# Performance work log

Hardware: AMD Instinct MI355X
Metric: run time of the kernel (lower is better)

The kernel has to match this reference:

```python
import jax, jax.numpy as jnp
import numpy as np

B, C, IMG, P = 32, 3, 224, 16
D, H, L, F, NCLS = 768, 12, 12, 3072, 1000
NP = (IMG // P) ** 2  # 196
DH = D // H  # 64
EPS = 1e-5


def _ln(x, g, b):
    m = jnp.mean(x, axis=-1, keepdims=True)
    v = jnp.mean(jnp.square(x - m), axis=-1, keepdims=True)
    return (x - m) * jax.lax.rsqrt(v + EPS) * g + b


def setup_inputs() -> dict:
    key = jax.random.key(0)
    ks = iter(jax.random.split(key, 32))
    s = 0.02
    rn = lambda shape: jax.random.normal(next(ks), shape, dtype=jnp.float32) * s
    inp = {
        "x": jax.random.normal(next(ks), (B, C, IMG, IMG), dtype=jnp.float32),
        "Wp": rn((P * P * C, D)), "bp": jnp.zeros((D,), jnp.float32),
        "cls": rn((1, 1, D)), "pos": rn((1, NP + 1, D)),
        # per-layer stacked params (leading dim L)
        "ln1_g": jnp.ones((L, D), jnp.float32), "ln1_b": jnp.zeros((L, D), jnp.float32),
        "Wq": rn((L, H, D, DH)), "bq": jnp.zeros((L, H, DH), jnp.float32),
        "Wk": rn((L, H, D, DH)), "bk": jnp.zeros((L, H, DH), jnp.float32),
        "Wv": rn((L, H, D, DH)), "bv": jnp.zeros((L, H, DH), jnp.float32),
        "Wo": rn((L, D, D)), "bo": jnp.zeros((L, D), jnp.float32),
        "ln2_g": jnp.ones((L, D), jnp.float32), "ln2_b": jnp.zeros((L, D), jnp.float32),
        "W1": rn((L, D, F)), "b1": jnp.zeros((L, F), jnp.float32),
        "W2": rn((L, F, D)), "b2": jnp.zeros((L, D), jnp.float32),
        # classification head
        "hln_g": jnp.ones((D,), jnp.float32), "hln_b": jnp.zeros((D,), jnp.float32),
        "hW1": rn((D, D)), "hb1": jnp.zeros((D,), jnp.float32),
        "hW2": rn((D, NCLS)), "hb2": jnp.zeros((NCLS,), jnp.float32),
    }
    return inp


def _vit(x, Wp, bp, cls, pos, ln1_g, ln1_b, Wq, bq, Wk, bk, Wv, bv, Wo, bo,
         ln2_g, ln2_b, W1, b1, W2, b2, hln_g, hln_b, hW1, hb1, hW2, hb2):
    b = x.shape[0]
    g = IMG // P
    # nn.Unfold(k=16, s=16): channel order (c, kh, kw), patch order (ph, pw)
    patches = x.reshape(b, C, g, P, g, P).transpose(0, 2, 4, 1, 3, 5).reshape(b, NP, C * P * P)
    h = patches @ Wp + bp  # [b, NP, D]
    h = jnp.concatenate([jnp.broadcast_to(cls, (b, 1, D)), h], axis=1) + pos  # [b, S, D]

    scale = 1.0 / jnp.sqrt(jnp.asarray(DH, h.dtype))

    def step(h, p):
        g1, b1_, wq, bq_, wk, bk_, wv, bv_, wo, bo_, g2, b2_, w1, bb1, w2, bb2 = p
        xn = _ln(h, g1, b1_)
        q = jnp.einsum('bsd,hde->bhse', xn, wq) + bq_[:, None, :]
        k = jnp.einsum('bsd,hde->bhse', xn, wk) + bk_[:, None, :]
        v = jnp.einsum('bsd,hde->bhse', xn, wv) + bv_[:, None, :]
        scores = jnp.einsum('bhse,bhte->bhst', q, k) * scale
        attn = jax.nn.softmax(scores, axis=-1)
        o = jnp.einsum('bhst,bhte->bhse', attn, v)  # [b,H,S,DH]
        o = o.transpose(0, 2, 1, 3).reshape(b, -1, D)  # concat heads
        h = o @ wo + bo_ + h
        xn = _ln(h, g2, b2_)
        h = jax.nn.gelu(xn @ w1 + bb1, approximate=False) @ w2 + bb2 + h
        return h, None

    params = (ln1_g, ln1_b, Wq, bq, Wk, bk, Wv, bv, Wo, bo, ln2_g, ln2_b, W1, b1, W2, b2)
    h, _ = jax.lax.scan(step, h, params)

    c = h[:, 0, :]
    c = _ln(c, hln_g, hln_b)
    return jax.nn.gelu(c @ hW1 + hb1, approximate=False) @ hW2 + hb2


def reference(x, Wp, bp, cls, pos, ln1_g, ln1_b, Wq, bq, Wk, bk, Wv, bv, Wo, bo,
              ln2_g, ln2_b, W1, b1, W2, b2, hln_g, hln_b, hW1, hb1, hW2, hb2):
    return _vit(x, Wp, bp, cls, pos, ln1_g, ln1_b, Wq, bq, Wk, bk, Wv, bv, Wo, bo,
                ln2_g, ln2_b, W1, b1, W2, b2, hln_g, hln_b, hW1, hb1, hW2, hb2)
```

## Files before the change

### kernel.cpp

```cpp
#include <hip/hip_runtime.h>

typedef unsigned short u16;
typedef __attribute__((ext_vector_type(8))) short short8;
typedef __attribute__((ext_vector_type(4))) float f32x4;

#define NTOK 6304
#define SP 197

#define OFF_WQKVT 0L
#define OFF_WOT   42467328L
#define OFF_W1T   56623104L
#define OFF_W2T   113246208L
#define OFF_WPT   169869312L
#define OFF_BQKV  171048960L
#define OFF_H     171159552L
#define OFF_XN    190525440L
#define OFF_QKV   200208384L
#define OFF_SC    229257216L
#define OFF_PM1   288867840L
#define OFF_VT    327599616L
#define OFF_CN    340182528L
#define OFF_T1    340280832L
#define WS_NEEDED 340379136L

__device__ __forceinline__ u16 f2bf(float x) {
  unsigned int u = __float_as_uint(x);
  u += 0x7fffu + ((u >> 16) & 1u);
  return (u16)(u >> 16);
}

__device__ __forceinline__ float gelu_f(float x) {
  return 0.5f * x * (1.0f + erff(x * 0.70710678118654752f));
}

__device__ __forceinline__ void gload_lds16(const void* g, void* l) {
  __builtin_amdgcn_global_load_lds(
      (const __attribute__((address_space(1))) unsigned int*)g,
      (__attribute__((address_space(3))) unsigned int*)l, 16, 0, 0);
}

template <bool BIAS, bool GELU, bool RES, bool OBF16, bool REMAP>
__global__ __launch_bounds__(256, 3) void gemm_k(
    const u16* __restrict__ A, int lda,
    const u16* __restrict__ Bm, int ldb,
    void* Cv, int ldc,
    const float* __restrict__ bias, const float* res, int ldres,
    int M, int N, int K, int tilesN) {
  __shared__ float4 smemv[2048];
  char* smem = (char*)smemv;

  const int t = threadIdx.x;
  const int nwg = gridDim.x;
  const int orig = blockIdx.x;
  const int q8 = nwg >> 3, r8 = nwg & 7;
  const int xcd = orig & 7, loc = orig >> 3;
  const int wg =
      (xcd < r8 ? xcd * (q8 + 1) : r8 * (q8 + 1) + (xcd - r8) * q8) + loc;
  const int tn = wg % tilesN, tm = wg / tilesN;
  const int m0 = tm * 128, n0 = tn * 128;
  const int l = t & 63;
  const int lr = l & 15, kb = l >> 4;
  const int wr = (t >> 7) & 1, wc = (t >> 6) & 1;

  const f32x4 zf = {0.f, 0.f, 0.f, 0.f};
  f32x4 acc[4][4];
#pragma unroll
  for (int m = 0; m < 4; ++m)
#pragma unroll
    for (int n = 0; n < 4; ++n) acc[m][n] = zf;

  auto stage = [&](const u16* src, int ld, int row0, int maxrow, int k0,
                   char* ldsbase) {
#pragma unroll
    for (int p = 0; p < 4; ++p) {
      int idx = p * 256 + t;
      int r = idx >> 3;
      int cl = idx & 7;
      int cg = cl ^ (r & 7);
      int rr = row0 + r;
      rr = rr > maxrow ? maxrow : rr;
      gload_lds16(src + (long)rr * ld + k0 + cg * 8,
                  ldsbase + (long)(p * 256 + (t & ~63)) * 16);
    }
  };

  const int KT = K >> 6;
  for (int kt = 0; kt < KT; ++kt) {
    stage(A, lda, m0, M - 1, kt * 64, smem);
    stage(Bm, ldb, n0, N - 1, kt * 64, smem + 16384);
    __syncthreads();
    const char* Ab = smem;
    const char* Bb = smem + 16384;
#pragma unroll
    for (int kk = 0; kk < 2; ++kk) {
      const int cla = ((kk << 2) + kb) ^ (lr & 7);
      short8 af[4], bfv[4];
#pragma unroll
      for (int m = 0; m < 4; ++m)
        af[m] = *(const short8*)(Ab + ((wr * 64 + m * 16 + lr) * 128 + cla * 16));
#pragma unroll
      for (int n = 0; n < 4; ++n)
        bfv[n] = *(const short8*)(Bb + ((wc * 64 + n * 16 + lr) * 128 + cla * 16));
#pragma unroll
      for (int m = 0; m < 4; ++m)
#pragma unroll
        for (int n = 0; n < 4; ++n)
          acc[m][n] = __builtin_amdgcn_mfma_f32_16x16x32_bf16(af[m], bfv[n],
                                                              acc[m][n], 0, 0, 0);
    }
    __syncthreads();
  }

#pragma unroll
  for (int n = 0; n < 4; ++n) {
    const int gc = n0 + wc * 64 + n * 16 + lr;
    if (gc >= N) continue;
    const float bv = BIAS ? bias[gc] : 0.0f;
#pragma unroll
    for (int m = 0; m < 4; ++m) {
#pragma unroll
      for (int j = 0; j < 4; ++j) {
        const int gr = m0 + wr * 64 + m * 16 + kb * 4 + j;
        if (gr >= M) continue;
        float v = acc[m][n][j] + bv;
        if (RES) v += res[(long)gr * ldres + gc];
        if (GELU) v = gelu_f(v);
        long orow = gr;
        if (REMAP) orow = (long)(gr / 196) * 197 + (gr % 196) + 1;
        if (OBF16)
          ((u16*)Cv)[orow * (long)ldc + gc] = f2bf(v);
        else
          ((float*)Cv)[orow * (long)ldc + gc] = v;
      }
    }
  }
}

template <int BM, int BN, int WM, int WN, bool BIAS, bool GELU, bool RES,
          bool OBF16, bool REMAP>
__global__ __launch_bounds__(WM * WN * 64, 2) void gemm2(
    const u16* __restrict__ A, int lda,
    const u16* __restrict__ Bm, int ldb,
    void* Cv, int ldc,
    const float* __restrict__ bias, const float* res, int ldres,
    int M, int N, int K, int tilesN) {
  constexpr int THREADS = WM * WN * 64;
  constexpr int TM = BM / WM, TN = BN / WN;
  constexpr int FM = TM / 16, FN = TN / 16;
  constexpr int APT = (BM * 8) / THREADS;
  constexpr int BPT = (BN * 8) / THREADS;
  constexpr int ABYTES = BM * 128;
  constexpr int BUF = ABYTES + BN * 128;
  __shared__ __align__(16) char smem[2 * BUF];

  const int t = threadIdx.x;
  const int l = t & 63;
  const int lr = l & 15, kb = (l >> 4) & 3;
  const int wid = t >> 6;
  const int wr = wid / WN, wc = wid % WN;

  const int nwg = gridDim.x;
  const int orig = blockIdx.x;
  const int q8 = nwg >> 3, r8 = nwg & 7;
  const int xcd = orig & 7, loc = orig >> 3;
  const int wg =
      (xcd < r8 ? xcd * (q8 + 1) : r8 * (q8 + 1) + (xcd - r8) * q8) + loc;
  const int tn = wg % tilesN, tm = wg / tilesN;
  const int m0 = tm * BM, n0 = tn * BN;
  const int Mm1 = M - 1, Nm1 = N - 1;

  const f32x4 zf = {0.f, 0.f, 0.f, 0.f};
  f32x4 acc[FM][FN];
#pragma unroll
  for (int fm = 0; fm < FM; ++fm)
#pragma unroll
    for (int fn = 0; fn < FN; ++fn) acc[fm][fn] = zf;

  auto stage = [&](int kt, int d) {
    const int k0 = kt << 6;
    char* base = smem + d * BUF;
#pragma unroll
    for (int p = 0; p < APT; ++p) {
      int idx = p * THREADS + t;
      int r = idx >> 3, cl = idx & 7;
      int rr = m0 + r;
      rr = rr > Mm1 ? Mm1 : rr;
      gload_lds16(A + (long)rr * lda + k0 + ((cl ^ (r & 7)) << 3),
                  base + ((p * THREADS + (t & ~63)) << 4));
    }
    char* bbase = base + ABYTES;
#pragma unroll
    for (int p = 0; p < BPT; ++p) {
      int idx = p * THREADS + t;
      int r = idx >> 3, cl = idx & 7;
      int rr = n0 + r;
      rr = rr > Nm1 ? Nm1 : rr;
      gload_lds16(Bm + (long)rr * ldb + k0 + ((cl ^ (r & 7)) << 3),
                  bbase + ((p * THREADS + (t & ~63)) << 4));
    }
  };

  const int nt = K >> 6;
  stage(0, 0);
  __syncthreads();

  for (int kt = 0; kt < nt; ++kt) {
    if (kt + 1 < nt) stage(kt + 1, (kt + 1) & 1);
    const char* Ab = smem + (kt & 1) * BUF;
    const char* Bb = Ab + ABYTES;
#pragma unroll
    for (int kk = 0; kk < 2; ++kk) {
      const int ch = ((((kk << 2) | kb) ^ (lr & 7)) << 4);
      short8 af[FM], bf[FN];
#pragma unroll
      for (int fm = 0; fm < FM; ++fm)
        af[fm] = *(const short8*)(Ab + (wr * TM + fm * 16 + lr) * 128 + ch);
#pragma unroll
      for (int fn = 0; fn < FN; ++fn)
        bf[fn] = *(const short8*)(Bb + (wc * TN + fn * 16 + lr) * 128 + ch);
#pragma unroll
      for (int fm = 0; fm < FM; ++fm)
#pragma unroll
        for (int fn = 0; fn < FN; ++fn)
          acc[fm][fn] = __builtin_amdgcn_mfma_f32_16x16x32_bf16(af[fm], bf[fn],
                                                                acc[fm][fn], 0, 0, 0);
    }
    __syncthreads();
  }

#pragma unroll
  for (int fn = 0; fn < FN; ++fn) {
    const int gc = n0 + wc * TN + fn * 16 + lr;
    if (gc >= N) continue;
    const float bv = BIAS ? bias[gc] : 0.0f;
#pragma unroll
    for (int fm = 0; fm < FM; ++fm) {
#pragma unroll
      for (int j = 0; j < 4; ++j) {
        const int gr = m0 + wr * TM + fm * 16 + kb * 4 + j;
        if (gr >= M) continue;
        float v = acc[fm][fn][j] + bv;
        if (RES) v += res[(long)gr * ldres + gc];
        if (GELU) v = gelu_f(v);
        long orow = gr;
        if (REMAP) orow = (long)(gr / 196) * 197 + (gr % 196) + 1;
        if (OBF16)
          ((u16*)Cv)[orow * (long)ldc + gc] = f2bf(v);
        else
          ((float*)Cv)[orow * (long)ldc + gc] = v;
      }
    }
  }
}

__global__ __launch_bounds__(256) void k_attn(const u16* __restrict__ qkv,
                                              u16* __restrict__ o) {
  __shared__ __align__(16) u16 Kb[208 * 72];
  __shared__ __align__(16) u16 Vt[64 * 232];
  __shared__ __align__(16) u16 Pl[4][16 * 232];

  const int t = threadIdx.x;
  const int z = blockIdx.x;
  const int b = z / 12, hh = z % 12;
  const long qbase = (long)b * SP * 2304 + hh * 64;

#pragma unroll
  for (int p = 0; p < 7; ++p) {
    int idx = p * 256 + t;
    int row = idx >> 3, c = idx & 7;
    short8 kv = {0, 0, 0, 0, 0, 0, 0, 0};
    short8 vv = {0, 0, 0, 0, 0, 0, 0, 0};
    if (row < SP) {
      kv = *(const short8*)(qkv + qbase + 768 + (long)row * 2304 + c * 8);
      vv = *(const short8*)(qkv + qbase + 1536 + (long)row * 2304 + c * 8);
    }
    if (row < 208) *(short8*)(&Kb[row * 72 + c * 8]) = kv;
#pragma unroll
    for (int j = 0; j < 8; ++j) Vt[(c * 8 + j) * 232 + row] = ((const u16*)&vv)[j];
  }
  __syncthreads();

  const int l = t & 63, wid = t >> 6;
  const int lr = l & 15, kb = l >> 4;
  u16* Pw = Pl[wid];
  const f32x4 zf = {0.f, 0.f, 0.f, 0.f};

  for (int st = wid; st < 13; st += 4) {
    int qrow = st * 16 + lr;
    qrow = qrow > SP - 1 ? SP - 1 : qrow;
    short8 qf[2];
#pragma unroll
    for (int kk = 0; kk < 2; ++kk)
      qf[kk] = *(const short8*)(qkv + qbase + (long)qrow * 2304 + kk * 32 + kb * 8);

    f32x4 s[13];
#pragma unroll
    for (int nt = 0; nt < 13; ++nt) {
      s[nt] = zf;
#pragma unroll
      for (int kk = 0; kk < 2; ++kk) {
        short8 kf = *(const short8*)(&Kb[(nt * 16 + lr) * 72 + kk * 32 + kb * 8]);
        s[nt] = __builtin_amdgcn_mfma_f32_16x16x32_bf16(qf[kk], kf, s[nt], 0, 0, 0);
      }
    }

    float mx[4] = {-1e30f, -1e30f, -1e30f, -1e30f};
#pragma unroll
    for (int nt = 0; nt < 13; ++nt) {
      const bool pred = (nt < 12) | (lr < 5);
#pragma unroll
      for (int j = 0; j < 4; ++j) {
        float v = s[nt][j] * 0.125f;
        s[nt][j] = v;
        if (pred) mx[j] = fmaxf(mx[j], v);
      }
    }
#pragma unroll
    for (int o4 = 1; o4 < 16; o4 <<= 1)
#pragma unroll
      for (int j = 0; j < 4; ++j) mx[j] = fmaxf(mx[j], __shfl_xor(mx[j], o4));
    float sum[4] = {0.f, 0.f, 0.f, 0.f};
#pragma unroll
    for (int nt = 0; nt < 13; ++nt) {
      const bool pred = (nt < 12) | (lr < 5);
#pragma unroll
      for (int j = 0; j < 4; ++j) {
        float p = pred ? __expf(s[nt][j] - mx[j]) : 0.f;
        s[nt][j] = p;
        sum[j] += p;
      }
    }
#pragma unroll
    for (int o4 = 1; o4 < 16; o4 <<= 1)
#pragma unroll
      for (int j = 0; j < 4; ++j) sum[j] += __shfl_xor(sum[j], o4);
    float inv[4];
#pragma unroll
    for (int j = 0; j < 4; ++j) inv[j] = 1.0f / sum[j];

#pragma unroll
    for (int nt = 0; nt < 13; ++nt)
#pragma unroll
      for (int j = 0; j < 4; ++j)
        Pw[(kb * 4 + j) * 232 + nt * 16 + lr] = f2bf(s[nt][j] * inv[j]);
#pragma unroll
    for (int j = 0; j < 4; ++j) Pw[(kb * 4 + j) * 232 + 208 + lr] = 0;

    short8 pf[7];
#pragma unroll
    for (int kk = 0; kk < 7; ++kk)
      pf[kk] = *(const short8*)(&Pw[lr * 232 + kk * 32 + kb * 8]);
#pragma unroll
    for (int dt = 0; dt < 4; ++dt) {
      f32x4 oacc = zf;
#pragma unroll
      for (int kk = 0; kk < 7; ++kk) {
        short8 vf = *(const short8*)(&Vt[(dt * 16 + lr) * 232 + kk * 32 + kb * 8]);
        oacc = __builtin_amdgcn_mfma_f32_16x16x32_bf16(pf[kk], vf, oacc, 0, 0, 0);
      }
#pragma unroll
      for (int j = 0; j < 4; ++j) {
        int qr = st * 16 + kb * 4 + j;
        if (qr < SP)
          o[((long)b * SP + qr) * 768 + hh * 64 + dt * 16 + lr] = f2bf(oacc[j]);
      }
    }
  }
}

__global__ void k_wt64(const float* __restrict__ W, u16* __restrict__ out,
                       int sel) {
  __shared__ float tile[32][33];
  const int z = blockIdx.z;
  const int ly = z / 12, hh = z % 12;
  const float* ip = W + (long)z * 768 * 64;
  u16* op = out + (long)ly * 2304 * 768 + ((long)sel * 768 + hh * 64) * 768;
  const int c0 = blockIdx.x * 32, r0 = blockIdx.y * 32;
  const int tx = threadIdx.x, ty = threadIdx.y;
#pragma unroll
  for (int i = 0; i < 4; ++i)
    tile[ty + i * 8][tx] = ip[(long)(r0 + ty + i * 8) * 64 + c0 + tx];
  __syncthreads();
#pragma unroll
  for (int i = 0; i < 4; ++i)
    op[(long)(c0 + ty + i * 8) * 768 + r0 + tx] = f2bf(tile[tx][ty + i * 8]);
}

__global__ void k_bqkv(const float* __restrict__ bq, const float* __restrict__ bk,
                       const float* __restrict__ bv, float* __restrict__ out) {
  int idx = blockIdx.x * 256 + threadIdx.x;
  if (idx >= 27648) return;
  int c = idx % 2304, ly = idx / 2304;
  int sel = c / 768, cc = c % 768;
  const float* b = sel == 0 ? bq : (sel == 1 ? bk : bv);
  out[idx] = b[ly * 768 + cc];
}

__global__ void k_transpose(const float* __restrict__ in, u16* __restrict__ out,
                            int R, int C) {
  __shared__ float tile[32][33];
  long zoff = (long)blockIdx.z * R * C;
  const float* ip = in + zoff;
  u16* op = out + zoff;
  int c0 = blockIdx.x * 32, r0 = blockIdx.y * 32;
  int tx = threadIdx.x, ty = threadIdx.y;
#pragma unroll
  for (int i = 0; i < 4; ++i)
    tile[ty + i * 8][tx] = ip[(long)(r0 + ty + i * 8) * C + c0 + tx];
  __syncthreads();
#pragma unroll
  for (int i = 0; i < 4; ++i)
    op[(long)(c0 + ty + i * 8) * R + r0 + tx] = f2bf(tile[tx][ty + i * 8]);
}

__global__ void k_patchify(const float* __restrict__ x, u16* __restrict__ out) {
  long idx = (long)blockIdx.x * 256 + threadIdx.x;
  int f = (int)(idx % 768);
  long rp = idx / 768;
  int p = (int)(rp % 196), b = (int)(rp / 196);
  int gy = p / 14, gx = p % 14;
  int c = f >> 8, rem = f & 255;
  int i = rem >> 4, j = rem & 15;
  out[idx] = f2bf(x[(((long)b * 3 + c) * 224 + gy * 16 + i) * 224 + gx * 16 + j]);
}

__global__ void k_add_pos(float* h, const float* __restrict__ cls,
                          const float* __restrict__ pos) {
  long idx = (long)blockIdx.x * 256 + threadIdx.x;
  int d4 = (int)(idx % 192);
  long rs = idx / 192;
  int s = (int)(rs % 197);
  float4* hp = (float4*)h;
  const float4* pp = (const float4*)pos;
  if (s == 0) {
    const float4* cp = (const float4*)cls;
    float4 v = cp[d4], w = pp[d4];
    v.x += w.x; v.y += w.y; v.z += w.z; v.w += w.w;
    hp[idx] = v;
  } else {
    float4 v = hp[idx], w = pp[(long)s * 192 + d4];
    v.x += w.x; v.y += w.y; v.z += w.z; v.w += w.w;
    hp[idx] = v;
  }
}

__global__ __launch_bounds__(256) void k_ln(const float* __restrict__ in,
                                            const float* __restrict__ g,
                                            const float* __restrict__ b,
                                            u16* __restrict__ out, int rows) {
  int w = threadIdx.x >> 6, l = threadIdx.x & 63;
  int row = blockIdx.x * 4 + w;
  if (row >= rows) return;
  const float4* ip = (const float4*)(in + (long)row * 768);
  float4 v[3];
  float s = 0.f, sq = 0.f;
#pragma unroll
  for (int i = 0; i < 3; ++i) {
    v[i] = ip[i * 64 + l];
    s += v[i].x + v[i].y + v[i].z + v[i].w;
    sq += v[i].x * v[i].x + v[i].y * v[i].y + v[i].z * v[i].z + v[i].w * v[i].w;
  }
#pragma unroll
  for (int o = 1; o < 64; o <<= 1) {
    s += __shfl_xor(s, o);
    sq += __shfl_xor(sq, o);
  }
  const float m = s * (1.f / 768.f);
  const float rs = rsqrtf(sq * (1.f / 768.f) - m * m + 1e-5f);
  ushort4* op = (ushort4*)(out + (long)row * 768);
#pragma unroll
  for (int i = 0; i < 3; ++i) {
    int c4 = (i * 64 + l) * 4;
    float4 gv = *(const float4*)(g + c4);
    float4 bv = *(const float4*)(b + c4);
    ushort4 o4;
    o4.x = f2bf((v[i].x - m) * rs * gv.x + bv.x);
    o4.y = f2bf((v[i].y - m) * rs * gv.y + bv.y);
    o4.z = f2bf((v[i].z - m) * rs * gv.z + bv.z);
    o4.w = f2bf((v[i].w - m) * rs * gv.w + bv.w);
    op[i * 64 + l] = o4;
  }
}

__global__ void k_head_ln(const float* __restrict__ h, const float* __restrict__ g,
                          const float* __restrict__ b, float* __restrict__ out) {
  const int bb = blockIdx.x, l = threadIdx.x;
  const float4* ip = (const float4*)(h + (long)bb * 197 * 768);
  float4 v[3];
  float s = 0.f, sq = 0.f;
#pragma unroll
  for (int i = 0; i < 3; ++i) {
    v[i] = ip[i * 64 + l];
    s += v[i].x + v[i].y + v[i].z + v[i].w;
    sq += v[i].x * v[i].x + v[i].y * v[i].y + v[i].z * v[i].z + v[i].w * v[i].w;
  }
#pragma unroll
  for (int o = 1; o < 64; o <<= 1) {
    s += __shfl_xor(s, o);
    sq += __shfl_xor(sq, o);
  }
  const float m = s * (1.f / 768.f);
  const float rs = rsqrtf(sq * (1.f / 768.f) - m * m + 1e-5f);
  float4* op = (float4*)(out + bb * 768);
#pragma unroll
  for (int i = 0; i < 3; ++i) {
    int c4 = (i * 64 + l) * 4;
    float4 gv = *(const float4*)(g + c4);
    float4 bv = *(const float4*)(b + c4);
    float4 o4;
    o4.x = (v[i].x - m) * rs * gv.x + bv.x;
    o4.y = (v[i].y - m) * rs * gv.y + bv.y;
    o4.z = (v[i].z - m) * rs * gv.z + bv.z;
    o4.w = (v[i].w - m) * rs * gv.w + bv.w;
    op[i * 64 + l] = o4;
  }
}

template <bool GELU>
__global__ __launch_bounds__(256) void k_head_gemm(
    const float* __restrict__ in, const float* __restrict__ W,
    const float* __restrict__ bias, float* __restrict__ out, int K, int N) {
  __shared__ float partial[4][64];
  const int b = blockIdx.y;
  const int cl = threadIdx.x & 63;
  const int c = blockIdx.x * 64 + cl;
  const int kp = threadIdx.x >> 6;
  const int kc = K >> 2;
  float s = 0.f;
  if (c < N) {
    const float* ip = in + (long)b * K + kp * kc;
    const float* wp = W + (long)(kp * kc) * N + c;
    for (int k = 0; k < kc; ++k) s = fmaf(ip[k], wp[(long)k * N], s);
  }
  partial[kp][cl] = s;
  __syncthreads();
  if (kp == 0 && c < N) {
    float v = partial[0][cl] + partial[1][cl] + partial[2][cl] + partial[3][cl] +
              bias[c];
    if (GELU) v = gelu_f(v);
    out[(long)b * N + c] = v;
  }
}

extern "C" void kernel_launch(void* const* d_in, const int* in_sizes, int n_in,
                              void* d_out, int out_size, void* d_ws, size_t ws_size,
                              hipStream_t stream) {
  (void)in_sizes; (void)n_in; (void)out_size;
  if ((long)ws_size < WS_NEEDED) return;

  const float* x = (const float*)d_in[0];
  const float* Wp = (const float*)d_in[1];
  const float* bp = (const float*)d_in[2];
  const float* cls = (const float*)d_in[3];
  const float* pos = (const float*)d_in[4];
  const float* ln1g = (const float*)d_in[5];
  const float* ln1b = (const float*)d_in[6];
  const float* Wq = (const float*)d_in[7];
  const float* bq = (const float*)d_in[8];
  const float* Wk = (const float*)d_in[9];
  const float* bk = (const float*)d_in[10];
  const float* Wv = (const float*)d_in[11];
  const float* bv = (const float*)d_in[12];
  const float* Wo = (const float*)d_in[13];
  const float* bo = (const float*)d_in[14];
  const float* ln2g = (const float*)d_in[15];
  const float* ln2b = (const float*)d_in[16];
  const float* W1 = (const float*)d_in[17];
  const float* b1 = (const float*)d_in[18];
  const float* W2 = (const float*)d_in[19];
  const float* b2 = (const float*)d_in[20];
  const float* hlng = (const float*)d_in[21];
  const float* hlnb = (const float*)d_in[22];
  const float* hW1 = (const float*)d_in[23];
  const float* hb1 = (const float*)d_in[24];
  const float* hW2 = (const float*)d_in[25];
  const float* hb2 = (const float*)d_in[26];

  char* ws = (char*)d_ws;
  u16* wqkvt = (u16*)(ws + OFF_WQKVT);
  u16* wot = (u16*)(ws + OFF_WOT);
  u16* w1t = (u16*)(ws + OFF_W1T);
  u16* w2t = (u16*)(ws + OFF_W2T);
  u16* wpt = (u16*)(ws + OFF_WPT);
  float* bqkv = (float*)(ws + OFF_BQKV);
  float* h = (float*)(ws + OFF_H);
  u16* xn = (u16*)(ws + OFF_XN);
  u16* qkv = (u16*)(ws + OFF_QKV);
  u16* pbuf = qkv;
  u16* m1 = (u16*)(ws + OFF_PM1);
  float* cn = (float*)(ws + OFF_CN);
  float* t1 = (float*)(ws + OFF_T1);

  k_wt64<<<dim3(2, 24, 144), dim3(32, 8), 0, stream>>>(Wq, wqkvt, 0);
  k_wt64<<<dim3(2, 24, 144), dim3(32, 8), 0, stream>>>(Wk, wqkvt, 1);
  k_wt64<<<dim3(2, 24, 144), dim3(32, 8), 0, stream>>>(Wv, wqkvt, 2);
  k_bqkv<<<108, 256, 0, stream>>>(bq, bk, bv, bqkv);
  k_transpose<<<dim3(24, 24, 12), dim3(32, 8), 0, stream>>>(Wo, wot, 768, 768);
  k_transpose<<<dim3(96, 24, 12), dim3(32, 8), 0, stream>>>(W1, w1t, 768, 3072);
  k_transpose<<<dim3(24, 96, 12), dim3(32, 8), 0, stream>>>(W2, w2t, 3072, 768);
  k_transpose<<<dim3(24, 24, 1), dim3(32, 8), 0, stream>>>(Wp, wpt, 768, 768);

  k_patchify<<<18816, 256, 0, stream>>>(x, pbuf);
  gemm2<128, 128, 2, 2, true, false, false, false, true><<<294, 256, 0, stream>>>(
      pbuf, 768, wpt, 768, h, 768, bp, nullptr, 0, 6272, 768, 768, 6);
  k_add_pos<<<4728, 256, 0, stream>>>(h, cls, pos);

  for (int ly = 0; ly < 12; ++ly) {
    k_ln<<<1576, 256, 0, stream>>>(h, ln1g + ly * 768, ln1b + ly * 768, xn, NTOK);
    gemm_k<true, false, false, true, false><<<900, 256, 0, stream>>>(
        xn, 768, wqkvt + (long)ly * 2304 * 768, 768, qkv, 2304,
        bqkv + ly * 2304, nullptr, 0, NTOK, 2304, 768, 18);
    k_attn<<<384, 256, 0, stream>>>(qkv, xn);
    gemm2<128, 128, 2, 2, true, false, true, false, false><<<300, 256, 0, stream>>>(
        xn, 768, wot + (long)ly * 768 * 768, 768, h, 768,
        bo + ly * 768, h, 768, NTOK, 768, 768, 6);
    k_ln<<<1576, 256, 0, stream>>>(h, ln2g + ly * 768, ln2b + ly * 768, xn, NTOK);
    gemm_k<true, true, false, true, false><<<1200, 256, 0, stream>>>(
        xn, 768, w1t + (long)ly * 3072 * 768, 768, m1, 3072,
        b1 + ly * 3072, nullptr, 0, NTOK, 3072, 768, 24);
    gemm2<128, 128, 2, 2, true, false, true, false, false><<<300, 256, 0, stream>>>(
        m1, 3072, w2t + (long)ly * 768 * 3072, 3072, h, 768,
        b2 + ly * 768, h, 768, NTOK, 768, 3072, 6);
  }

  k_head_ln<<<32, 64, 0, stream>>>(h, hlng, hlnb, cn);
  k_head_gemm<true><<<dim3(12, 32), 256, 0, stream>>>(cn, hW1, hb1, t1, 768, 768);
  k_head_gemm<false><<<dim3(16, 32), 256, 0, stream>>>(t1, hW2, hb2, (float*)d_out,
                                                       768, 1000);
}
```

Baseline: 3.260 ms.

## Widen QKV and FC1 GEMM tiles to 256x128 with 512-thread blocks

Replaces the 128x128, 256-thread GEMM used for the QKV and FC1 projections with a 256x128 tile computed by 8 waves (512 threads). The B tile is now staged once per workgroup and shared by two rows of waves, so global-to-LDS traffic for the weight operand per unit of output drops. LDS use per block grows to 48KB and the grid halves, which lowers the number of blocks and can leave more padding waste on the M edge (6304 rows into 256-row tiles).

```diff
diff --git a/kernel.cpp b/kernel.cpp
--- a/kernel.cpp
+++ b/kernel.cpp
@@ -40,16 +40,21 @@
 }
 
 template <bool BIAS, bool GELU, bool RES, bool OBF16, bool REMAP>
-__global__ __launch_bounds__(256, 3) void gemm_k(
+__global__ __launch_bounds__(512, 2) void gemm_w(
     const u16* __restrict__ A, int lda,
     const u16* __restrict__ Bm, int ldb,
     void* Cv, int ldc,
     const float* __restrict__ bias, const float* res, int ldres,
     int M, int N, int K, int tilesN) {
-  __shared__ float4 smemv[2048];
-  char* smem = (char*)smemv;
+  __shared__ __align__(16) char smem[49152];
 
   const int t = threadIdx.x;
+  const int l = t & 63;
+  const int lr = l & 15, kb = (l >> 4) & 3;
+  const int wid = t >> 6;
+  const int wr = wid >> 1;
+  const int wc = wid & 1;
+
   const int nwg = gridDim.x;
   const int orig = blockIdx.x;
   const int q8 = nwg >> 3, r8 = nwg & 7;
@@ -57,10 +62,8 @@
   const int wg =
       (xcd < r8 ? xcd * (q8 + 1) : r8 * (q8 + 1) + (xcd - r8) * q8) + loc;
   const int tn = wg % tilesN, tm = wg / tilesN;
-  const int m0 = tm * 128, n0 = tn * 128;
-  const int l = t & 63;
-  const int lr = l & 15, kb = l >> 4;
-  const int wr = (t >> 7) & 1, wc = (t >> 6) & 1;
+  const int m0 = tm * 256, n0 = tn * 128;
+  const int Mm1 = M - 1, Nm1 = N - 1;
 
   const f32x4 zf = {0.f, 0.f, 0.f, 0.f};
   f32x4 acc[4][4];
@@ -69,38 +72,45 @@
 #pragma unroll
     for (int n = 0; n < 4; ++n) acc[m][n] = zf;
 
-  auto stage = [&](const u16* src, int ld, int row0, int maxrow, int k0,
-                   char* ldsbase) {
+  auto stage = [&](int k0) {
 #pragma unroll
     for (int p = 0; p < 4; ++p) {
-      int idx = p * 256 + t;
-      int r = idx >> 3;
-      int cl = idx & 7;
+      int idx = p * 512 + t;
+      int r = idx >> 3, cl = idx & 7;
       int cg = cl ^ (r & 7);
-      int rr = row0 + r;
-      rr = rr > maxrow ? maxrow : rr;
-      gload_lds16(src + (long)rr * ld + k0 + cg * 8,
-                  ldsbase + (long)(p * 256 + (t & ~63)) * 16);
+      int rr = m0 + r;
+      rr = rr > Mm1 ? Mm1 : rr;
+      gload_lds16(A + (long)rr * lda + k0 + cg * 8,
+                  smem + ((p * 512 + (t & ~63)) << 4));
+    }
+#pragma unroll
+    for (int p = 0; p < 2; ++p) {
+      int idx = p * 512 + t;
+      int r = idx >> 3, cl = idx & 7;
+      int cg = cl ^ (r & 7);
+      int rr = n0 + r;
+      rr = rr > Nm1 ? Nm1 : rr;
+      gload_lds16(Bm + (long)rr * ldb + k0 + cg * 8,
+                  smem + 32768 + ((p * 512 + (t & ~63)) << 4));
     }
   };
 
   const int KT = K >> 6;
   for (int kt = 0; kt < KT; ++kt) {
-    stage(A, lda, m0, M - 1, kt * 64, smem);
-    stage(Bm, ldb, n0, N - 1, kt * 64, smem + 16384);
+    stage(kt * 64);
     __syncthreads();
     const char* Ab = smem;
-    const char* Bb = smem + 16384;
+    const char* Bb = smem + 32768;
 #pragma unroll
     for (int kk = 0; kk < 2; ++kk) {
-      const int cla = ((kk << 2) + kb) ^ (lr & 7);
+      const int ch = ((((kk << 2) | kb) ^ (lr & 7)) << 4);
       short8 af[4], bfv[4];
 #pragma unroll
       for (int m = 0; m < 4; ++m)
-        af[m] = *(const short8*)(Ab + ((wr * 64 + m * 16 + lr) * 128 + cla * 16));
+        af[m] = *(const short8*)(Ab + (wr * 64 + m * 16 + lr) * 128 + ch);
 #pragma unroll
       for (int n = 0; n < 4; ++n)
-        bfv[n] = *(const short8*)(Bb + ((wc * 64 + n * 16 + lr) * 128 + cla * 16));
+        bfv[n] = *(const short8*)(Bb + (wc * 64 + n * 16 + lr) * 128 + ch);
 #pragma unroll
       for (int m = 0; m < 4; ++m)
 #pragma unroll
@@ -607,7 +617,7 @@
 
   for (int ly = 0; ly < 12; ++ly) {
     k_ln<<<1576, 256, 0, stream>>>(h, ln1g + ly * 768, ln1b + ly * 768, xn, NTOK);
-    gemm_k<true, false, false, true, false><<<900, 256, 0, stream>>>(
+    gemm_w<true, false, false, true, false><<<450, 512, 0, stream>>>(
         xn, 768, wqkvt + (long)ly * 2304 * 768, 768, qkv, 2304,
         bqkv + ly * 2304, nullptr, 0, NTOK, 2304, 768, 18);
     k_attn<<<384, 256, 0, stream>>>(qkv, xn);
@@ -615,7 +625,7 @@
         xn, 768, wot + (long)ly * 768 * 768, 768, h, 768,
         bo + ly * 768, h, 768, NTOK, 768, 768, 6);
     k_ln<<<1576, 256, 0, stream>>>(h, ln2g + ly * 768, ln2b + ly * 768, xn, NTOK);
-    gemm_k<true, true, false, true, false><<<1200, 256, 0, stream>>>(
+    gemm_w<true, true, false, true, false><<<600, 512, 0, stream>>>(
         xn, 768, w1t + (long)ly * 3072 * 768, 768, m1, 3072,
         b1 + ly * 3072, nullptr, 0, NTOK, 3072, 768, 24);
     gemm2<128, 128, 2, 2, true, false, true, false, false><<<300, 256, 0, stream>>>(
```

Result: no change. 3.285 ms (+0.8%).
